# Kernel optimization log

Hardware: AMD Instinct MI355X
Metric: run time of the kernel (lower is better)

Reference implementation:

```python
import jax, jax.numpy as jnp
import numpy as np

N, E, DIM, HEADS = 50000, 600000, 128, 4
C = DIM // HEADS  # per-head channels = 32
NEG_SLOPE = 0.2
LN_EPS = 1e-5


def setup_inputs() -> dict:
    key = jax.random.key(0)
    ks = jax.random.split(key, 6)
    x = jax.random.normal(ks[0], (N, DIM), dtype=jnp.float32)
    edge_index = jax.random.randint(ks[1], (2, E), 0, N, dtype=jnp.int32)
    W = jax.random.normal(ks[2], (DIM, DIM), dtype=jnp.float32) / np.sqrt(DIM).astype(np.float32)
    b = jnp.zeros((DIM,), jnp.float32)
    att_src = jax.random.normal(ks[3], (HEADS, C), dtype=jnp.float32) * 0.1
    att_dst = jax.random.normal(ks[4], (HEADS, C), dtype=jnp.float32) * 0.1
    gamma = jnp.ones((DIM,), jnp.float32)
    beta = jnp.zeros((DIM,), jnp.float32)
    return {"x": x, "W": W, "b": b, "att_src": att_src, "att_dst": att_dst,
            "gamma": gamma, "beta": beta, "edge_index": edge_index}


def _gat_conv(x, W, b, att_src, att_dst, src, dst):
    # linear projection, per-head view: [N, H, C]
    h = (x @ W).reshape(N, HEADS, C)
    # per-node attention logits: [N, H]
    a_s = jnp.einsum('nhc,hc->nh', h, att_src)
    a_d = jnp.einsum('nhc,hc->nh', h, att_dst)
    # per-edge logits with leaky relu: [Etot, H]
    e = jax.nn.leaky_relu(a_s[src] + a_d[dst], negative_slope=NEG_SLOPE)
    # segment softmax over incoming edges of each dst node
    m = jax.ops.segment_max(e, dst, num_segments=N)
    ez = jnp.exp(e - m[dst])
    denom = jax.ops.segment_sum(ez, dst, num_segments=N) + 1e-16
    alpha = ez / denom[dst]  # [Etot, H]
    # weighted scatter-aggregation: [N, H, C]
    out = jax.ops.segment_sum(alpha[:, :, None] * h[src], dst, num_segments=N)
    return out.reshape(N, DIM) + b


def reference(x, W, b, att_src, att_dst, gamma, beta, edge_index):
    # add self loops (PyG GATConv default add_self_loops=True)
    loops = jnp.arange(N, dtype=edge_index.dtype)
    src = jnp.concatenate([edge_index[0], loops])
    dst = jnp.concatenate([edge_index[1], loops])
    g = _gat_conv(x, W, b, att_src, att_dst, src, dst)
    # residual + GELU (torch exact erf GELU) + LayerNorm; dropout = identity (eval)
    y = x + jax.nn.gelu(g, approximate=False)
    mu = jnp.mean(y, axis=-1, keepdims=True)
    var = jnp.mean(jnp.square(y - mu), axis=-1, keepdims=True)
    return (y - mu) / jnp.sqrt(var + LN_EPS) * gamma + beta
```

## Files before the change

kernel.cpp:

```cpp
#include <hip/hip_runtime.h>
#include <math.h>

#define DIMC 128
#define HEADSC 4

typedef __attribute__((ext_vector_type(8))) short bf16x8;
typedef __attribute__((ext_vector_type(4))) float f32x4;
typedef __attribute__((ext_vector_type(2))) float f32x2;

static __device__ __forceinline__ float bf2f(unsigned short u) {
    unsigned v = ((unsigned)u) << 16;
    return __builtin_bit_cast(float, v);
}
static __device__ __forceinline__ short f2bf(float f) {
    unsigned u = __builtin_bit_cast(unsigned, f);
    unsigned r = (u + 0x7fff + ((u >> 16) & 1)) >> 16;
    return (short)r;
}
static __device__ __forceinline__ float blo(unsigned q) {
    return __builtin_bit_cast(float, q << 16);
}
static __device__ __forceinline__ float bhi(unsigned q) {
    return __builtin_bit_cast(float, q & 0xffff0000u);
}

__global__ __launch_bounds__(256) void gemm_kernel(
    const float* __restrict__ x, const float* __restrict__ W,
    const float* __restrict__ att_src, const float* __restrict__ att_dst,
    unsigned short* __restrict__ hb, float* __restrict__ a_s, float* __restrict__ a_d,
    int* __restrict__ counts, int N, int nstrip)
{
    for (int idx = blockIdx.x * 256 + threadIdx.x; idx < N; idx += gridDim.x * 256)
        counts[idx] = 0;

    const int lane = threadIdx.x & 63;
    const int wv   = threadIdx.x >> 6;
    const int pr   = wv >> 1;
    const int half = wv & 1;
    const int l15  = lane & 15;
    const int lg   = lane >> 4;

    bf16x8 bfr[4][4];
#pragma unroll
    for (int ct = 0; ct < 4; ++ct) {
#pragma unroll
        for (int kk = 0; kk < 4; ++kk) {
            const float* wp = W + (size_t)(kk * 32 + lg * 8) * DIMC + half * 64 + ct * 16 + l15;
#pragma unroll
            for (int jj = 0; jj < 8; ++jj)
                bfr[ct][kk][jj] = f2bf(wp[(size_t)jj * DIMC]);
        }
    }
    float attS[4], attD[4];
#pragma unroll
    for (int ct = 0; ct < 4; ++ct) {
        attS[ct] = att_src[half * 64 + ct * 16 + l15];
        attD[ct] = att_dst[half * 64 + ct * 16 + l15];
    }

    for (int s = blockIdx.x * 2 + pr; s < nstrip; s += gridDim.x * 2) {
        const int row = s * 16 + l15;
        const float* xp = x + (size_t)row * DIMC + lg * 8;
        bf16x8 afr[4];
#pragma unroll
        for (int kk = 0; kk < 4; ++kk) {
            f32x4 v0 = *(const f32x4*)(xp + kk * 32);
            f32x4 v1 = *(const f32x4*)(xp + kk * 32 + 4);
#pragma unroll
            for (int jj = 0; jj < 4; ++jj) {
                afr[kk][jj]     = f2bf(v0[jj]);
                afr[kk][jj + 4] = f2bf(v1[jj]);
            }
        }
        f32x4 acc[4] = {};
#pragma unroll
        for (int ct = 0; ct < 4; ++ct) {
#pragma unroll
            for (int kk = 0; kk < 4; ++kk)
                acc[ct] = __builtin_amdgcn_mfma_f32_16x16x32_bf16(
                    afr[kk], bfr[ct][kk], acc[ct], 0, 0, 0);
        }
        unsigned short* hp = hb + (size_t)(s * 16) * DIMC + half * 64;
#pragma unroll
        for (int ct = 0; ct < 4; ++ct)
#pragma unroll
            for (int reg = 0; reg < 4; ++reg)
                hp[(size_t)(lg * 4 + reg) * DIMC + ct * 16 + l15] =
                    (unsigned short)f2bf(acc[ct][reg]);
#pragma unroll
        for (int reg = 0; reg < 4; ++reg) {
            float s0 = fmaf(acc[0][reg], attS[0], acc[1][reg] * attS[1]);
            float s1 = fmaf(acc[2][reg], attS[2], acc[3][reg] * attS[3]);
            float d0 = fmaf(acc[0][reg], attD[0], acc[1][reg] * attD[1]);
            float d1 = fmaf(acc[2][reg], attD[2], acc[3][reg] * attD[3]);
#pragma unroll
            for (int mk = 1; mk < 16; mk <<= 1) {
                s0 += __shfl_xor(s0, mk);
                s1 += __shfl_xor(s1, mk);
                d0 += __shfl_xor(d0, mk);
                d1 += __shfl_xor(d1, mk);
            }
            if (l15 == 0) {
                const int r = s * 16 + lg * 4 + reg;
                a_s[r * HEADSC + half * 2 + 0] = s0;
                a_s[r * HEADSC + half * 2 + 1] = s1;
                a_d[r * HEADSC + half * 2 + 0] = d0;
                a_d[r * HEADSC + half * 2 + 1] = d1;
            }
        }
    }
}

__global__ void hist_kernel(const int* __restrict__ dst, int E, int* __restrict__ counts)
{
    int i = blockIdx.x * blockDim.x + threadIdx.x;
    int stride = gridDim.x * blockDim.x;
    for (; i < E; i += stride) atomicAdd(&counts[dst[i]], 1);
}

__global__ __launch_bounds__(256) void scan1_kernel(
    const int* __restrict__ counts, int* __restrict__ partial, int N)
{
    const int t = threadIdx.x, i = blockIdx.x * 256 + t;
    int v = (i < N) ? counts[i] + 1 : 0;
    int s = v;
#pragma unroll
    for (int mk = 1; mk < 64; mk <<= 1) s += __shfl_xor(s, mk);
    __shared__ int ws[4];
    if ((t & 63) == 0) ws[t >> 6] = s;
    __syncthreads();
    if (t == 0) partial[blockIdx.x] = ws[0] + ws[1] + ws[2] + ws[3];
}

__global__ __launch_bounds__(256) void scan2_kernel(
    int* __restrict__ partial, int* __restrict__ offsets, int P, int N)
{
    const int t = threadIdx.x;
    const int lane = t & 63, wv = t >> 6;
    int v = (t < P) ? partial[t] : 0;
    int xs = v;
#pragma unroll
    for (int d = 1; d < 64; d <<= 1) {
        int tt = __shfl_up(xs, d);
        if (lane >= d) xs += tt;
    }
    __shared__ int ws[4], wo[4];
    if (lane == 63) ws[wv] = xs;
    __syncthreads();
    if (t == 0) {
        int s = 0;
        for (int w = 0; w < 4; ++w) { wo[w] = s; s += ws[w]; }
        offsets[N] = s;
    }
    __syncthreads();
    if (t < P) partial[t] = wo[wv] + xs - v;
}

__global__ __launch_bounds__(256) void scan3_kernel(
    const int* __restrict__ counts, const int* __restrict__ partial,
    int* __restrict__ offsets, int* __restrict__ cursor, int N)
{
    const int t = threadIdx.x, i = blockIdx.x * 256 + t;
    const int lane = t & 63, wv = t >> 6;
    int v = (i < N) ? counts[i] + 1 : 0;
    int xs = v;
#pragma unroll
    for (int d = 1; d < 64; d <<= 1) {
        int tt = __shfl_up(xs, d);
        if (lane >= d) xs += tt;
    }
    __shared__ int ws[4], wo[4];
    if (lane == 63) ws[wv] = xs;
    __syncthreads();
    if (t == 0) {
        int s = 0;
        for (int w = 0; w < 4; ++w) { wo[w] = s; s += ws[w]; }
    }
    __syncthreads();
    const int excl = partial[blockIdx.x] + wo[wv] + xs - v;
    if (i < N) { offsets[i] = excl; cursor[i] = excl; }
}

__global__ void scatter_kernel(const int* __restrict__ ei, int E, int N,
                               const float* __restrict__ a_s,
                               const float* __restrict__ a_d,
                               int* __restrict__ cursor, int* __restrict__ rec,
                               float* __restrict__ pexp)
{
    int i = blockIdx.x * blockDim.x + threadIdx.x;
    const int total = E + N;
    const int stride = gridDim.x * blockDim.x;
    for (; i < total; i += stride) {
        int s, d;
        if (i < E) { s = ei[i]; d = ei[E + i]; }
        else       { s = i - E; d = s; }
        const int pos = atomicAdd(&cursor[d], 1);
        rec[pos] = s;
        const f32x4 as = *(const f32x4*)(a_s + (size_t)s * HEADSC);
        const f32x4 ad = *(const f32x4*)(a_d + (size_t)d * HEADSC);
        f32x4 p;
#pragma unroll
        for (int h = 0; h < HEADSC; ++h) {
            float e = as[h] + ad[h];
            e = (e > 0.f) ? e : 0.2f * e;
            p[h] = __expf(e);
        }
        *(f32x4*)(pexp + (size_t)pos * HEADSC) = p;
    }
}

__global__ __launch_bounds__(256) void node_kernel(
    const float* __restrict__ x, const unsigned short* __restrict__ hb,
    const int* __restrict__ offsets, const int* __restrict__ rec,
    const float* __restrict__ pexp,
    const float* __restrict__ bias, const float* __restrict__ gamma,
    const float* __restrict__ beta, float* __restrict__ out, int N)
{
    const int wv = threadIdx.x >> 6;
    const int lane = threadIdx.x & 63;
    const int c2 = lane * 2;
    const int head = lane >> 4;

    for (int n = blockIdx.x * 4 + wv; n < N; n += gridDim.x * 4) {
        const int beg = __builtin_amdgcn_readfirstlane(offsets[n]);
        const int end = __builtin_amdgcn_readfirstlane(offsets[n + 1]);
        float den = 0.f, e0 = 0.f, e1 = 0.f, o0 = 0.f, o1 = 0.f;
        int i = beg;
        const int e4 = beg + ((end - beg) & ~3);
        for (; i < e4; i += 4) {
            const int s0 = rec[i + 0], s1 = rec[i + 1];
            const int s2 = rec[i + 2], s3 = rec[i + 3];
            const float p0 = pexp[(size_t)(i + 0) * HEADSC + head];
            const float p1 = pexp[(size_t)(i + 1) * HEADSC + head];
            const float p2 = pexp[(size_t)(i + 2) * HEADSC + head];
            const float p3 = pexp[(size_t)(i + 3) * HEADSC + head];
            const unsigned q0 = *(const unsigned*)(hb + (size_t)s0 * DIMC + c2);
            const unsigned q1 = *(const unsigned*)(hb + (size_t)s1 * DIMC + c2);
            const unsigned q2 = *(const unsigned*)(hb + (size_t)s2 * DIMC + c2);
            const unsigned q3 = *(const unsigned*)(hb + (size_t)s3 * DIMC + c2);
            den += (p0 + p1) + (p2 + p3);
            e0 = fmaf(p0, blo(q0), e0); e1 = fmaf(p0, bhi(q0), e1);
            o0 = fmaf(p1, blo(q1), o0); o1 = fmaf(p1, bhi(q1), o1);
            e0 = fmaf(p2, blo(q2), e0); e1 = fmaf(p2, bhi(q2), e1);
            o0 = fmaf(p3, blo(q3), o0); o1 = fmaf(p3, bhi(q3), o1);
        }
        for (; i < end; ++i) {
            const int s0 = rec[i];
            const float p0 = pexp[(size_t)i * HEADSC + head];
            const unsigned q0 = *(const unsigned*)(hb + (size_t)s0 * DIMC + c2);
            den += p0;
            e0 = fmaf(p0, blo(q0), e0);
            e1 = fmaf(p0, bhi(q0), e1);
        }
        const float acc0 = e0 + o0, acc1 = e1 + o1;

        const float inv = 1.f / (den + 1e-16f);
        const f32x2 bi = *(const f32x2*)(bias + c2);
        float g0 = acc0 * inv + bi.x;
        float g1 = acc1 * inv + bi.y;
        const float ge0 = 0.5f * g0 * (1.f + erff(g0 * 0.70710678118654752f));
        const float ge1 = 0.5f * g1 * (1.f + erff(g1 * 0.70710678118654752f));
        const f32x2 xv = *(const f32x2*)(x + (size_t)n * DIMC + c2);
        const float y0 = xv.x + ge0;
        const float y1 = xv.y + ge1;
        float s1 = y0 + y1, s2 = y0 * y0 + y1 * y1;
#pragma unroll
        for (int mk = 1; mk < 64; mk <<= 1) {
            s1 += __shfl_xor(s1, mk);
            s2 += __shfl_xor(s2, mk);
        }
        const float mu = s1 * (1.f / DIMC);
        const float var = s2 * (1.f / DIMC) - mu * mu;
        const float rstd = rsqrtf(var + 1e-5f);
        const f32x2 ga = *(const f32x2*)(gamma + c2);
        const f32x2 be = *(const f32x2*)(beta + c2);
        f32x2 o;
        o.x = (y0 - mu) * rstd * ga.x + be.x;
        o.y = (y1 - mu) * rstd * ga.y + be.y;
        *(f32x2*)(out + (size_t)n * DIMC + c2) = o;
    }
}

extern "C" void kernel_launch(void* const* d_in, const int* in_sizes, int n_in,
                              void* d_out, int out_size, void* d_ws, size_t ws_size,
                              hipStream_t stream)
{
    const float* x       = (const float*)d_in[0];
    const float* W       = (const float*)d_in[1];
    const float* bias    = (const float*)d_in[2];
    const float* att_src = (const float*)d_in[3];
    const float* att_dst = (const float*)d_in[4];
    const float* gamma   = (const float*)d_in[5];
    const float* beta    = (const float*)d_in[6];
    const int*   ei      = (const int*)d_in[7];

    const int N = in_sizes[0] / DIMC;
    const int E = in_sizes[7] / 2;

    unsigned short* hb = (unsigned short*)d_ws;
    float* a_s   = (float*)(hb + (size_t)N * DIMC);
    float* a_d   = a_s + (size_t)N * HEADSC;
    float* pexp  = a_d + (size_t)N * HEADSC;
    int* counts  = (int*)(pexp + (size_t)(E + N) * HEADSC);
    int* offsets = counts + N;
    int* cursor  = offsets + N + 1;
    int* partial = cursor + N;
    int* rec     = partial + 256;

    const int nstrip = (N + 15) / 16;
    gemm_kernel<<<784, 256, 0, stream>>>(x, W, att_src, att_dst, hb, a_s, a_d,
                                         counts, N, nstrip);
    hist_kernel<<<2048, 256, 0, stream>>>(ei + E, E, counts);
    const int nb1 = (N + 255) / 256;
    scan1_kernel<<<nb1, 256, 0, stream>>>(counts, partial, N);
    scan2_kernel<<<1, 256, 0, stream>>>(partial, offsets, nb1, N);
    scan3_kernel<<<nb1, 256, 0, stream>>>(counts, partial, offsets, cursor, N);
    scatter_kernel<<<2048, 256, 0, stream>>>(ei, E, N, a_s, a_d, cursor, rec, pexp);
    node_kernel<<<(N + 3) / 4, 256, 0, stream>>>(
        x, hb, offsets, rec, pexp, bias, gamma, beta, (float*)d_out, N);
}
```

Before: 205.3 us.

## Fuse histogram into GEMM, merge scans, recompute edge exps in node kernel

The degree histogram moves into the tail of the GEMM kernel, and counts are now zeroed with a memset. The two-level offset scan is merged into one kernel that recomputes block prefixes from the partial sums. Once the scatter has run, the cursor array itself holds end offsets. The scatter now writes only source indices, reading edges as int4 vectors, and the per-edge pexp buffer is removed. The node kernel instead recomputes the leaky-relu exp from a_s/a_d, trading extra gathers and exps for less global write and read traffic and fewer launches.

```diff
diff --git a/kernel.cpp b/kernel.cpp
--- a/kernel.cpp
+++ b/kernel.cpp
@@ -8,10 +8,6 @@
 typedef __attribute__((ext_vector_type(4))) float f32x4;
 typedef __attribute__((ext_vector_type(2))) float f32x2;
 
-static __device__ __forceinline__ float bf2f(unsigned short u) {
-    unsigned v = ((unsigned)u) << 16;
-    return __builtin_bit_cast(float, v);
-}
 static __device__ __forceinline__ short f2bf(float f) {
     unsigned u = __builtin_bit_cast(unsigned, f);
     unsigned r = (u + 0x7fff + ((u >> 16) & 1)) >> 16;
@@ -24,15 +20,13 @@
     return __builtin_bit_cast(float, q & 0xffff0000u);
 }
 
-__global__ __launch_bounds__(256) void gemm_kernel(
+__global__ __launch_bounds__(256) void gemm_hist_kernel(
     const float* __restrict__ x, const float* __restrict__ W,
     const float* __restrict__ att_src, const float* __restrict__ att_dst,
+    const int* __restrict__ dst, int E,
     unsigned short* __restrict__ hb, float* __restrict__ a_s, float* __restrict__ a_d,
     int* __restrict__ counts, int N, int nstrip)
 {
-    for (int idx = blockIdx.x * 256 + threadIdx.x; idx < N; idx += gridDim.x * 256)
-        counts[idx] = 0;
-
     const int lane = threadIdx.x & 63;
     const int wv   = threadIdx.x >> 6;
     const int pr   = wv >> 1;
@@ -109,13 +103,21 @@
             }
         }
     }
-}
-
-__global__ void hist_kernel(const int* __restrict__ dst, int E, int* __restrict__ counts)
-{
-    int i = blockIdx.x * blockDim.x + threadIdx.x;
-    int stride = gridDim.x * blockDim.x;
-    for (; i < E; i += stride) atomicAdd(&counts[dst[i]], 1);
+
+    const int tid = blockIdx.x * 256 + threadIdx.x;
+    const int stride = gridDim.x * 256;
+    if (((E & 3) == 0) && ((((size_t)dst) & 15) == 0)) {
+        const int E4 = E >> 2;
+        for (int i = tid; i < E4; i += stride) {
+            const int4 d4 = ((const int4*)dst)[i];
+            atomicAdd(&counts[d4.x], 1);
+            atomicAdd(&counts[d4.y], 1);
+            atomicAdd(&counts[d4.z], 1);
+            atomicAdd(&counts[d4.w], 1);
+        }
+    } else {
+        for (int i = tid; i < E; i += stride) atomicAdd(&counts[dst[i]], 1);
+    }
 }
 
 __global__ __launch_bounds__(256) void scan1_kernel(
@@ -132,87 +134,71 @@
     if (t == 0) partial[blockIdx.x] = ws[0] + ws[1] + ws[2] + ws[3];
 }
 
-__global__ __launch_bounds__(256) void scan2_kernel(
-    int* __restrict__ partial, int* __restrict__ offsets, int P, int N)
+__global__ __launch_bounds__(256) void scan23_kernel(
+    const int* __restrict__ counts, const int* __restrict__ partial,
+    int* __restrict__ S, int N, int P)
 {
     const int t = threadIdx.x;
     const int lane = t & 63, wv = t >> 6;
-    int v = (t < P) ? partial[t] : 0;
-    int xs = v;
-#pragma unroll
-    for (int d = 1; d < 64; d <<= 1) {
-        int tt = __shfl_up(xs, d);
-        if (lane >= d) xs += tt;
-    }
-    __shared__ int ws[4], wo[4];
+    __shared__ int ws[4];
+    __shared__ int ex[256];
+
+    int pv = (t < P) ? partial[t] : 0;
+    int xs = pv;
+#pragma unroll
+    for (int d = 1; d < 64; d <<= 1) { int tt = __shfl_up(xs, d); if (lane >= d) xs += tt; }
     if (lane == 63) ws[wv] = xs;
     __syncthreads();
-    if (t == 0) {
-        int s = 0;
-        for (int w = 0; w < 4; ++w) { wo[w] = s; s += ws[w]; }
-        offsets[N] = s;
-    }
-    __syncthreads();
-    if (t < P) partial[t] = wo[wv] + xs - v;
-}
-
-__global__ __launch_bounds__(256) void scan3_kernel(
-    const int* __restrict__ counts, const int* __restrict__ partial,
-    int* __restrict__ offsets, int* __restrict__ cursor, int N)
-{
-    const int t = threadIdx.x, i = blockIdx.x * 256 + t;
-    const int lane = t & 63, wv = t >> 6;
+    int wof = 0;
+#pragma unroll
+    for (int w = 0; w < 4; ++w) wof += (w < wv) ? ws[w] : 0;
+    ex[t] = wof + xs - pv;
+    __syncthreads();
+    const int prefix = ex[blockIdx.x];
+    __syncthreads();
+
+    const int i = blockIdx.x * 256 + t;
     int v = (i < N) ? counts[i] + 1 : 0;
-    int xs = v;
-#pragma unroll
-    for (int d = 1; d < 64; d <<= 1) {
-        int tt = __shfl_up(xs, d);
-        if (lane >= d) xs += tt;
-    }
-    __shared__ int ws[4], wo[4];
-    if (lane == 63) ws[wv] = xs;
-    __syncthreads();
-    if (t == 0) {
-        int s = 0;
-        for (int w = 0; w < 4; ++w) { wo[w] = s; s += ws[w]; }
-    }
-    __syncthreads();
-    const int excl = partial[blockIdx.x] + wo[wv] + xs - v;
-    if (i < N) { offsets[i] = excl; cursor[i] = excl; }
+    int s2 = v;
+#pragma unroll
+    for (int d = 1; d < 64; d <<= 1) { int tt = __shfl_up(s2, d); if (lane >= d) s2 += tt; }
+    if (lane == 63) ws[wv] = s2;
+    __syncthreads();
+    int wof2 = 0;
+#pragma unroll
+    for (int w = 0; w < 4; ++w) wof2 += (w < wv) ? ws[w] : 0;
+    if (i < N) S[i] = prefix + wof2 + s2 - v;
 }
 
 __global__ void scatter_kernel(const int* __restrict__ ei, int E, int N,
-                               const float* __restrict__ a_s,
-                               const float* __restrict__ a_d,
-                               int* __restrict__ cursor, int* __restrict__ rec,
-                               float* __restrict__ pexp)
-{
-    int i = blockIdx.x * blockDim.x + threadIdx.x;
-    const int total = E + N;
+                               int* __restrict__ S, int* __restrict__ rec)
+{
+    const int tid = blockIdx.x * blockDim.x + threadIdx.x;
     const int stride = gridDim.x * blockDim.x;
-    for (; i < total; i += stride) {
-        int s, d;
-        if (i < E) { s = ei[i]; d = ei[E + i]; }
-        else       { s = i - E; d = s; }
-        const int pos = atomicAdd(&cursor[d], 1);
-        rec[pos] = s;
-        const f32x4 as = *(const f32x4*)(a_s + (size_t)s * HEADSC);
-        const f32x4 ad = *(const f32x4*)(a_d + (size_t)d * HEADSC);
-        f32x4 p;
-#pragma unroll
-        for (int h = 0; h < HEADSC; ++h) {
-            float e = as[h] + ad[h];
-            e = (e > 0.f) ? e : 0.2f * e;
-            p[h] = __expf(e);
-        }
-        *(f32x4*)(pexp + (size_t)pos * HEADSC) = p;
-    }
+    if (((E & 3) == 0) && ((((size_t)ei) & 15) == 0)) {
+        const int E4 = E >> 2;
+        const int4* s4p = (const int4*)ei;
+        const int4* d4p = (const int4*)(ei + E);
+        for (int i = tid; i < E4; i += stride) {
+            const int4 s4 = s4p[i];
+            const int4 d4 = d4p[i];
+            rec[atomicAdd(&S[d4.x], 1)] = s4.x;
+            rec[atomicAdd(&S[d4.y], 1)] = s4.y;
+            rec[atomicAdd(&S[d4.z], 1)] = s4.z;
+            rec[atomicAdd(&S[d4.w], 1)] = s4.w;
+        }
+    } else {
+        for (int i = tid; i < E; i += stride)
+            rec[atomicAdd(&S[ei[E + i]], 1)] = ei[i];
+    }
+    for (int n = tid; n < N; n += stride)
+        rec[atomicAdd(&S[n], 1)] = n;
 }
 
 __global__ __launch_bounds__(256) void node_kernel(
     const float* __restrict__ x, const unsigned short* __restrict__ hb,
-    const int* __restrict__ offsets, const int* __restrict__ rec,
-    const float* __restrict__ pexp,
+    const int* __restrict__ S, const int* __restrict__ rec,
+    const float* __restrict__ a_s, const float* __restrict__ a_d,
     const float* __restrict__ bias, const float* __restrict__ gamma,
     const float* __restrict__ beta, float* __restrict__ out, int N)
 {
@@ -222,22 +208,29 @@
     const int head = lane >> 4;
 
     for (int n = blockIdx.x * 4 + wv; n < N; n += gridDim.x * 4) {
-        const int beg = __builtin_amdgcn_readfirstlane(offsets[n]);
-        const int end = __builtin_amdgcn_readfirstlane(offsets[n + 1]);
+        const int beg = __builtin_amdgcn_readfirstlane(n ? S[n - 1] : 0);
+        const int end = __builtin_amdgcn_readfirstlane(S[n]);
+        const float adh = a_d[n * HEADSC + head];
         float den = 0.f, e0 = 0.f, e1 = 0.f, o0 = 0.f, o1 = 0.f;
         int i = beg;
         const int e4 = beg + ((end - beg) & ~3);
         for (; i < e4; i += 4) {
             const int s0 = rec[i + 0], s1 = rec[i + 1];
             const int s2 = rec[i + 2], s3 = rec[i + 3];
-            const float p0 = pexp[(size_t)(i + 0) * HEADSC + head];
-            const float p1 = pexp[(size_t)(i + 1) * HEADSC + head];
-            const float p2 = pexp[(size_t)(i + 2) * HEADSC + head];
-            const float p3 = pexp[(size_t)(i + 3) * HEADSC + head];
+            float t0 = a_s[s0 * HEADSC + head] + adh;
+            float t1 = a_s[s1 * HEADSC + head] + adh;
+            float t2 = a_s[s2 * HEADSC + head] + adh;
+            float t3 = a_s[s3 * HEADSC + head] + adh;
             const unsigned q0 = *(const unsigned*)(hb + (size_t)s0 * DIMC + c2);
             const unsigned q1 = *(const unsigned*)(hb + (size_t)s1 * DIMC + c2);
             const unsigned q2 = *(const unsigned*)(hb + (size_t)s2 * DIMC + c2);
             const unsigned q3 = *(const unsigned*)(hb + (size_t)s3 * DIMC + c2);
+            t0 = (t0 > 0.f) ? t0 : 0.2f * t0;
+            t1 = (t1 > 0.f) ? t1 : 0.2f * t1;
+            t2 = (t2 > 0.f) ? t2 : 0.2f * t2;
+            t3 = (t3 > 0.f) ? t3 : 0.2f * t3;
+            const float p0 = __expf(t0), p1 = __expf(t1);
+            const float p2 = __expf(t2), p3 = __expf(t3);
             den += (p0 + p1) + (p2 + p3);
             e0 = fmaf(p0, blo(q0), e0); e1 = fmaf(p0, bhi(q0), e1);
             o0 = fmaf(p1, blo(q1), o0); o1 = fmaf(p1, bhi(q1), o1);
@@ -246,8 +239,10 @@
         }
         for (; i < end; ++i) {
             const int s0 = rec[i];
-            const float p0 = pexp[(size_t)i * HEADSC + head];
+            float t0 = a_s[s0 * HEADSC + head] + adh;
             const unsigned q0 = *(const unsigned*)(hb + (size_t)s0 * DIMC + c2);
+            t0 = (t0 > 0.f) ? t0 : 0.2f * t0;
+            const float p0 = __expf(t0);
             den += p0;
             e0 = fmaf(p0, blo(q0), e0);
             e1 = fmaf(p0, bhi(q0), e1);
@@ -300,22 +295,20 @@
     unsigned short* hb = (unsigned short*)d_ws;
     float* a_s   = (float*)(hb + (size_t)N * DIMC);
     float* a_d   = a_s + (size_t)N * HEADSC;
-    float* pexp  = a_d + (size_t)N * HEADSC;
-    int* counts  = (int*)(pexp + (size_t)(E + N) * HEADSC);
-    int* offsets = counts + N;
-    int* cursor  = offsets + N + 1;
-    int* partial = cursor + N;
+    int* counts  = (int*)(a_d + (size_t)N * HEADSC);
+    int* S       = counts + N;
+    int* partial = S + N;
     int* rec     = partial + 256;
 
+    hipMemsetAsync(counts, 0, sizeof(int) * (size_t)N, stream);
+
     const int nstrip = (N + 15) / 16;
-    gemm_kernel<<<784, 256, 0, stream>>>(x, W, att_src, att_dst, hb, a_s, a_d,
-                                         counts, N, nstrip);
-    hist_kernel<<<2048, 256, 0, stream>>>(ei + E, E, counts);
+    gemm_hist_kernel<<<784, 256, 0, stream>>>(x, W, att_src, att_dst, ei + E, E,
+                                              hb, a_s, a_d, counts, N, nstrip);
     const int nb1 = (N + 255) / 256;
     scan1_kernel<<<nb1, 256, 0, stream>>>(counts, partial, N);
-    scan2_kernel<<<1, 256, 0, stream>>>(partial, offsets, nb1, N);
-    scan3_kernel<<<nb1, 256, 0, stream>>>(counts, partial, offsets, cursor, N);
-    scatter_kernel<<<2048, 256, 0, stream>>>(ei, E, N, a_s, a_d, cursor, rec, pexp);
+    scan23_kernel<<<nb1, 256, 0, stream>>>(counts, partial, S, N, nb1);
+    scatter_kernel<<<640, 256, 0, stream>>>(ei, E, N, S, rec);
     node_kernel<<<(N + 3) / 4, 256, 0, stream>>>(
-        x, hb, offsets, rec, pexp, bias, gamma, beta, (float*)d_out, N);
-}
+        x, hb, S, rec, a_s, a_d, bias, gamma, beta, (float*)d_out, N);
+}
```

After: 200.2 us. 1.03x faster.
